# Performance work log

Measured on AMD Instinct MI355X. Metric: run time of the kernel, lower is better.

The kernel has to match this reference:

```python
import jax, jax.numpy as jnp
import numpy as np

N, D, R, B, K = 16384, 300, 10, 1024, 64


def setup_inputs() -> dict:
    key = jax.random.key(0)
    ks = jax.random.split(key, 6)
    return {
        "node_feat_src": jax.random.normal(ks[0], (N, D), jnp.float32),
        "node_feat_tgt": jax.random.normal(ks[1], (N, D), jnp.float32),
        "srcs_index": jax.random.randint(ks[2], (B, K), 0, N),
        "tgts_index": jax.random.randint(ks[3], (B, K), 0, N),
        "src_vs": jax.random.normal(ks[4], (R, D), jnp.float32),
        "tgt_vs": jax.random.normal(ks[5], (R, D), jnp.float32),
    }


def _tower(h, vs):
    # Householder chain: h @ (I - v v^T / (v^T v)) == h - ((h v) / (v^T v)) v^T
    def step(h, v):
        coef = (h @ v) / (v @ v)  # [N]
        return h - coef[:, None] * v[None, :], None
    h, _ = jax.lax.scan(step, h, vs)
    return h


def _l2norm(x):
    # matches F.normalize(p=2, eps=1e-12) over the last dim
    n = jnp.linalg.norm(x, axis=-1, keepdims=True)
    return x / jnp.maximum(n, 1e-12)


def reference(node_feat_src, node_feat_tgt, srcs_index, tgts_index, src_vs, tgt_vs):
    src_h = _tower(node_feat_src, src_vs)  # [N, D]
    tgt_h = _tower(node_feat_tgt, tgt_vs)  # [N, D]

    pos_src = _l2norm(src_h[srcs_index[:, 0]])  # [B, D]
    pos_tgt = _l2norm(tgt_h[tgts_index[:, 0]])  # [B, D]
    src_list = _l2norm(src_h[srcs_index])       # [B, K, D]
    tgt_list = _l2norm(tgt_h[tgts_index])       # [B, K, D]

    sim_src2tgt = jnp.einsum('bd,bkd->bk', pos_src, tgt_list)  # [B, K]
    sim_tgt2src = jnp.einsum('bd,bkd->bk', pos_tgt, src_list)  # [B, K]

    # CSLS hubness penalties: mean of top-10 cross-domain cosine sims
    sim_matrix = _l2norm(src_h) @ _l2norm(tgt_h).T  # [N, N]
    rt = jnp.mean(jax.lax.top_k(sim_matrix, 10)[0], axis=1)    # [N]
    rs = jnp.mean(jax.lax.top_k(sim_matrix.T, 10)[0], axis=1)  # [N]

    srcs_rt = rt[srcs_index]  # [B, K]
    tgts_rs = rs[tgts_index]  # [B, K]

    logits_src2tgt = sim_src2tgt * 2 - srcs_rt[:, 0:1] - tgts_rs
    logits_tgt2src = sim_tgt2src * 2 - tgts_rs[:, 0:1] - srcs_rt
    return logits_src2tgt, logits_tgt2src
```

## Files before the change

kernel.cpp:

```cpp
#include <hip/hip_runtime.h>
#include <hip/hip_bf16.h>

#define NN 16384
#define DD 300
#define DP 320
#define RR 10
#define BB 1024
#define KK 64
#define CAP 128
#define CAPL 1024

typedef __attribute__((ext_vector_type(8))) short s8v;
typedef __attribute__((ext_vector_type(4))) float f4v;
typedef _Float16 h2 __attribute__((ext_vector_type(2)));

__device__ __forceinline__ unsigned mono2(unsigned d) {
    unsigned s = ((d >> 15) & 0x10001u) * 0xFFFFu;
    return d ^ (s | 0x80008000u);
}
__device__ __forceinline__ float key2f16(unsigned k) {
    unsigned short b = (k & 0x8000u) ? (unsigned short)(k ^ 0x8000u)
                                     : (unsigned short)(~k & 0xFFFFu);
    _Float16 hv = __builtin_bit_cast(_Float16, b);
    return (float)hv;
}

__device__ __forceinline__ h2 h2max(h2 a, h2 b) {
    return __builtin_elementwise_max(a, b);
}
__device__ __forceinline__ h2 hmax2s(h2 a, int xb) {
    int x = __shfl_xor(__builtin_bit_cast(int, a), xb);
    return h2max(a, __builtin_bit_cast(h2, x));
}
__device__ __forceinline__ h2 packh2(float a, float b) {
    h2 r; r[0] = (_Float16)a; r[1] = (_Float16)b; return r;
}

__device__ __forceinline__ void ins10(unsigned (&lst)[10], unsigned v) {
    #pragma unroll
    for (int q = 0; q < 10; ++q) {
        unsigned a  = lst[q];
        unsigned mx = a > v ? a : v;
        v           = a > v ? v : a;
        lst[q] = mx;
    }
}
__device__ __forceinline__ void ins10f(float (&lst)[10], float v) {
    #pragma unroll
    for (int q = 0; q < 10; ++q) {
        float a  = lst[q];
        float mx = fmaxf(a, v);
        v        = fminf(a, v);
        lst[q] = mx;
    }
}

__device__ __forceinline__ void xcd_map(int bid, int& by, int& bx) {
    const int xcd = bid & 7;
    const int s   = bid >> 3;
    bx = (xcd << 2) | (s & 3);
    by = s >> 2;
}

__global__ __launch_bounds__(256) void tower_kernel(
        const float* __restrict__ feat, const float* __restrict__ vs,
        __hip_bfloat16* __restrict__ out) {
    __shared__ float vsh[RR * DD];
    const int tid = threadIdx.x;
    for (int i = tid; i < RR * DD; i += 256) vsh[i] = vs[i];
    __syncthreads();

    const int lane = tid & 63;
    const int wave = tid >> 6;
    const int row  = blockIdx.x * 4 + wave;

    float h[5];
    #pragma unroll
    for (int j = 0; j < 5; ++j) {
        int d = lane + 64 * j;
        h[j] = (d < DD) ? feat[(size_t)row * DD + d] : 0.f;
    }
    #pragma unroll
    for (int r = 0; r < RR; ++r) {
        float vl[5];
        float hv = 0.f, vv = 0.f;
        #pragma unroll
        for (int j = 0; j < 5; ++j) {
            int d = lane + 64 * j;
            float v = (d < DD) ? vsh[r * DD + d] : 0.f;
            vl[j] = v;
            hv += h[j] * v;
            vv += v * v;
        }
        #pragma unroll
        for (int o = 32; o; o >>= 1) {
            hv += __shfl_xor(hv, o);
            vv += __shfl_xor(vv, o);
        }
        float coef = hv / vv;
        #pragma unroll
        for (int j = 0; j < 5; ++j) h[j] -= coef * vl[j];
    }
    float nn = 0.f;
    #pragma unroll
    for (int j = 0; j < 5; ++j) nn += h[j] * h[j];
    #pragma unroll
    for (int o = 32; o; o >>= 1) nn += __shfl_xor(nn, o);
    float scale = 1.f / fmaxf(sqrtf(nn), 1e-12f);
    #pragma unroll
    for (int j = 0; j < 5; ++j) {
        int d = lane + 64 * j;
        float val = (d < DD) ? h[j] * scale : 0.f;
        out[(size_t)row * DP + d] = __float2bfloat16(val);
    }
}

__global__ __launch_bounds__(512, 2) void passA_kernel(
        const __hip_bfloat16* __restrict__ A, const __hip_bfloat16* __restrict__ Bm,
        unsigned short* __restrict__ rowsmax_g,
        unsigned short* __restrict__ colsmax_g) {
    __shared__ __align__(16) char u_lds[32768];
    __shared__ unsigned short rowsm[16][512];
    __shared__ unsigned short colsm[512][16];

    __hip_bfloat16* Asub = (__hip_bfloat16*)u_lds;
    __hip_bfloat16* Bsub = (__hip_bfloat16*)(u_lds + 16384);

    const int tid = threadIdx.x;
    const int lane = tid & 63;
    const int w = tid >> 6, wr = w >> 2, wc = w & 3;
    int by, bx; xcd_map(blockIdx.x, by, bx);
    const int i0 = by * 512, j0 = bx * 512;

    const int sr0 = tid >> 3, su0 = tid & 7;
    const int sp0 = (su0 ^ (sr0 & 7)) * 8;

    for (int ti = 0; ti < 4; ++ti) {
        for (int tj = 0; tj < 4; ++tj) {
            f4v acc[4][2];
            #pragma unroll
            for (int m = 0; m < 4; ++m)
                #pragma unroll
                for (int n = 0; n < 2; ++n)
                    acc[m][n] = (f4v){0.f, 0.f, 0.f, 0.f};

            const __hip_bfloat16* Ab = A  + (size_t)(i0 + ti * 128) * DP;
            const __hip_bfloat16* Bb = Bm + (size_t)(j0 + tj * 128) * DP;

            size_t go = (size_t)sr0 * DP + su0 * 8;
            int4 va0 = *reinterpret_cast<const int4*>(Ab + go);
            int4 vb0 = *reinterpret_cast<const int4*>(Bb + go);
            int4 va1 = *reinterpret_cast<const int4*>(Ab + go + (size_t)64 * DP);
            int4 vb1 = *reinterpret_cast<const int4*>(Bb + go + (size_t)64 * DP);

            #pragma unroll
            for (int kb = 0; kb < 5; ++kb) {
                __syncthreads();
                *reinterpret_cast<int4*>(Asub + sr0 * 64 + sp0)        = va0;
                *reinterpret_cast<int4*>(Bsub + sr0 * 64 + sp0)        = vb0;
                *reinterpret_cast<int4*>(Asub + (sr0 + 64) * 64 + sp0) = va1;
                *reinterpret_cast<int4*>(Bsub + (sr0 + 64) * 64 + sp0) = vb1;
                __syncthreads();
                if (kb < 4) {
                    go += 64;
                    va0 = *reinterpret_cast<const int4*>(Ab + go);
                    vb0 = *reinterpret_cast<const int4*>(Bb + go);
                    va1 = *reinterpret_cast<const int4*>(Ab + go + (size_t)64 * DP);
                    vb1 = *reinterpret_cast<const int4*>(Bb + go + (size_t)64 * DP);
                }
                #pragma unroll
                for (int ks = 0; ks < 2; ++ks) {
                    s8v af[4], bfv[2];
                    const int ulog = ks * 4 + (lane >> 4);
                    const int up   = ulog ^ (lane & 7);
                    #pragma unroll
                    for (int m = 0; m < 4; ++m) {
                        const int row = wr * 64 + m * 16 + (lane & 15);
                        af[m] = *reinterpret_cast<const s8v*>(Asub + row * 64 + up * 8);
                    }
                    #pragma unroll
                    for (int n = 0; n < 2; ++n) {
                        const int row = wc * 32 + n * 16 + (lane & 15);
                        bfv[n] = *reinterpret_cast<const s8v*>(Bsub + row * 64 + up * 8);
                    }
                    #pragma unroll
                    for (int m = 0; m < 4; ++m)
                        #pragma unroll
                        for (int n = 0; n < 2; ++n)
                            acc[m][n] = __builtin_amdgcn_mfma_f32_16x16x32_bf16(
                                af[m], bfv[n], acc[m][n], 0, 0, 0);
                }
            }

            #pragma unroll
            for (int m = 0; m < 4; ++m) {
                h2 a01 = h2max(packh2(acc[m][0][0], acc[m][0][1]),
                               packh2(acc[m][1][0], acc[m][1][1]));
                h2 a23 = h2max(packh2(acc[m][0][2], acc[m][0][3]),
                               packh2(acc[m][1][2], acc[m][1][3]));
                a01 = hmax2s(a01, 1); a23 = hmax2s(a23, 1);
                a01 = hmax2s(a01, 2); a23 = hmax2s(a23, 2);
                a01 = hmax2s(a01, 4); a23 = hmax2s(a23, 4);
                a01 = hmax2s(a01, 8); a23 = hmax2s(a23, 8);
                if ((lane & 15) == m * 4) {
                    const int rl = ti * 128 + wr * 64 + m * 16 + ((lane >> 4) << 2);
                    uint2 u = make_uint2(mono2(__builtin_bit_cast(unsigned, a01)),
                                         mono2(__builtin_bit_cast(unsigned, a23)));
                    *reinterpret_cast<uint2*>(&rowsm[tj * 4 + wc][rl]) = u;
                }
            }
            float rm[4][2];
            #pragma unroll
            for (int m = 0; m < 4; ++m) {
                rm[m][0] = fmaxf(fmaxf(acc[m][0][0], acc[m][0][1]),
                                 fmaxf(acc[m][0][2], acc[m][0][3]));
                rm[m][1] = fmaxf(fmaxf(acc[m][1][0], acc[m][1][1]),
                                 fmaxf(acc[m][1][2], acc[m][1][3]));
            }
            h2 c0 = packh2(fmaxf(rm[0][0], rm[1][0]), fmaxf(rm[2][0], rm[3][0]));
            h2 c1 = packh2(fmaxf(rm[0][1], rm[1][1]), fmaxf(rm[2][1], rm[3][1]));
            c0 = hmax2s(c0, 16); c1 = hmax2s(c1, 16);
            c0 = hmax2s(c0, 32); c1 = hmax2s(c1, 32);
            if ((lane >> 4) == 0) {
                const int s = ti * 4 + wr * 2;
                const int cb = tj * 128 + wc * 32 + (lane & 15);
                *reinterpret_cast<unsigned*>(&colsm[cb][s])      = mono2(__builtin_bit_cast(unsigned, c0));
                *reinterpret_cast<unsigned*>(&colsm[cb + 16][s]) = mono2(__builtin_bit_cast(unsigned, c1));
            }
        }
    }
    __syncthreads();
    {
        const int r = tid;
        unsigned short t16[16];
        #pragma unroll
        for (int s = 0; s < 16; ++s) t16[s] = rowsm[s][r];
        uint4 o0, o1;
        o0.x = t16[0] | ((unsigned)t16[1] << 16);  o0.y = t16[2] | ((unsigned)t16[3] << 16);
        o0.z = t16[4] | ((unsigned)t16[5] << 16);  o0.w = t16[6] | ((unsigned)t16[7] << 16);
        o1.x = t16[8] | ((unsigned)t16[9] << 16);  o1.y = t16[10] | ((unsigned)t16[11] << 16);
        o1.z = t16[12] | ((unsigned)t16[13] << 16); o1.w = t16[14] | ((unsigned)t16[15] << 16);
        uint4* rdst = reinterpret_cast<uint4*>(rowsmax_g + (size_t)(i0 + r) * 512 + bx * 16);
        rdst[0] = o0; rdst[1] = o1;
        uint4 q0 = *reinterpret_cast<uint4*>(&colsm[r][0]);
        uint4 q1 = *reinterpret_cast<uint4*>(&colsm[r][8]);
        uint4* cdst = reinterpret_cast<uint4*>(colsmax_g + (size_t)(j0 + r) * 512 + by * 16);
        cdst[0] = q0; cdst[1] = q1;
    }
}

__global__ __launch_bounds__(256) void thresh_kernel(
        const unsigned short* __restrict__ rowsmax_g,
        const unsigned short* __restrict__ colsmax_g,
        float* __restrict__ Tlb_row, float* __restrict__ Tlb_col,
        unsigned* __restrict__ rowcnt, unsigned* __restrict__ colcnt) {
    const int t = blockIdx.x * 256 + threadIdx.x;
    const bool isRow = t < NN;
    const int idx = isRow ? t : t - NN;
    const unsigned short* src = (isRow ? rowsmax_g : colsmax_g) + (size_t)idx * 512;

    unsigned lst[10];
    #pragma unroll
    for (int q = 0; q < 10; ++q) lst[q] = 0u;

    const uint4* p = reinterpret_cast<const uint4*>(src);
    for (int c = 0; c < 64; ++c) {
        uint4 q = p[c];
        unsigned v0 = q.x & 0xFFFFu, v1 = q.x >> 16;
        unsigned v2 = q.y & 0xFFFFu, v3 = q.y >> 16;
        unsigned v4 = q.z & 0xFFFFu, v5 = q.z >> 16;
        unsigned v6 = q.w & 0xFFFFu, v7 = q.w >> 16;
        unsigned g01 = v0 > v1 ? v0 : v1, g23 = v2 > v3 ? v2 : v3;
        unsigned g45 = v4 > v5 ? v4 : v5, g67 = v6 > v7 ? v6 : v7;
        unsigned ga = g01 > g23 ? g01 : g23, gb = g45 > g67 ? g45 : g67;
        unsigned g = ga > gb ? ga : gb;
        if (g > lst[9]) {
            if (v0 > lst[9]) ins10(lst, v0);
            if (v1 > lst[9]) ins10(lst, v1);
            if (v2 > lst[9]) ins10(lst, v2);
            if (v3 > lst[9]) ins10(lst, v3);
            if (v4 > lst[9]) ins10(lst, v4);
            if (v5 > lst[9]) ins10(lst, v5);
            if (v6 > lst[9]) ins10(lst, v6);
            if (v7 > lst[9]) ins10(lst, v7);
        }
    }
    float f = key2f16(lst[9]);
    float lb = f - fabsf(f) * 0.002f - 1e-6f;
    if (isRow) { Tlb_row[idx] = lb; rowcnt[idx] = 0u; }
    else       { Tlb_col[idx] = lb; colcnt[idx] = 0u; }
}

__global__ __launch_bounds__(512, 2) void passB_kernel(
        const __hip_bfloat16* __restrict__ A, const __hip_bfloat16* __restrict__ Bm,
        const float* __restrict__ Tlb_row, const float* __restrict__ Tlb_col,
        unsigned* __restrict__ rowcnt, unsigned* __restrict__ colcnt,
        float* __restrict__ rowbuf, float* __restrict__ colbuf) {
    __shared__ __align__(16) char u_lds[32768];
    __shared__ float Trow_s[512];
    __shared__ float Tcol_s[512];
    __shared__ unsigned scnt[2];
    __shared__ uint2 sbuf[2][CAPL];

    __hip_bfloat16* Asub = (__hip_bfloat16*)u_lds;
    __hip_bfloat16* Bsub = (__hip_bfloat16*)(u_lds + 16384);

    const int tid = threadIdx.x;
    const int lane = tid & 63;
    const int w = tid >> 6, wr = w >> 2, wc = w & 3;
    int by, bx; xcd_map(blockIdx.x, by, bx);
    const int i0 = by * 512, j0 = bx * 512;

    Trow_s[tid] = Tlb_row[i0 + tid];
    Tcol_s[tid] = Tlb_col[j0 + tid];
    if (tid < 2) scnt[tid] = 0u;
    __syncthreads();

    const int sr0 = tid >> 3, su0 = tid & 7;
    const int sp0 = (su0 ^ (sr0 & 7)) * 8;

    for (int ti = 0; ti < 4; ++ti) {
        float trmin = 1e30f;
        #pragma unroll
        for (int m = 0; m < 4; ++m)
            #pragma unroll
            for (int r = 0; r < 4; ++r)
                trmin = fminf(trmin, Trow_s[ti * 128 + wr * 64 + m * 16 + ((lane >> 4) << 2) + r]);

        for (int tj = 0; tj < 4; ++tj) {
            f4v acc[4][2];
            #pragma unroll
            for (int m = 0; m < 4; ++m)
                #pragma unroll
                for (int n = 0; n < 2; ++n)
                    acc[m][n] = (f4v){0.f, 0.f, 0.f, 0.f};

            const __hip_bfloat16* Ab = A  + (size_t)(i0 + ti * 128) * DP;
            const __hip_bfloat16* Bb = Bm + (size_t)(j0 + tj * 128) * DP;

            size_t go = (size_t)sr0 * DP + su0 * 8;
            int4 va0 = *reinterpret_cast<const int4*>(Ab + go);
            int4 vb0 = *reinterpret_cast<const int4*>(Bb + go);
            int4 va1 = *reinterpret_cast<const int4*>(Ab + go + (size_t)64 * DP);
            int4 vb1 = *reinterpret_cast<const int4*>(Bb + go + (size_t)64 * DP);

            #pragma unroll
            for (int kb = 0; kb < 5; ++kb) {
                __syncthreads();
                *reinterpret_cast<int4*>(Asub + sr0 * 64 + sp0)        = va0;
                *reinterpret_cast<int4*>(Bsub + sr0 * 64 + sp0)        = vb0;
                *reinterpret_cast<int4*>(Asub + (sr0 + 64) * 64 + sp0) = va1;
                *reinterpret_cast<int4*>(Bsub + (sr0 + 64) * 64 + sp0) = vb1;
                __syncthreads();
                if (kb < 4) {
                    go += 64;
                    va0 = *reinterpret_cast<const int4*>(Ab + go);
                    vb0 = *reinterpret_cast<const int4*>(Bb + go);
                    va1 = *reinterpret_cast<const int4*>(Ab + go + (size_t)64 * DP);
                    vb1 = *reinterpret_cast<const int4*>(Bb + go + (size_t)64 * DP);
                }
                #pragma unroll
                for (int ks = 0; ks < 2; ++ks) {
                    s8v af[4], bfv[2];
                    const int ulog = ks * 4 + (lane >> 4);
                    const int up   = ulog ^ (lane & 7);
                    #pragma unroll
                    for (int m = 0; m < 4; ++m) {
                        const int row = wr * 64 + m * 16 + (lane & 15);
                        af[m] = *reinterpret_cast<const s8v*>(Asub + row * 64 + up * 8);
                    }
                    #pragma unroll
                    for (int n = 0; n < 2; ++n) {
                        const int row = wc * 32 + n * 16 + (lane & 15);
                        bfv[n] = *reinterpret_cast<const s8v*>(Bsub + row * 64 + up * 8);
                    }
                    #pragma unroll
                    for (int m = 0; m < 4; ++m)
                        #pragma unroll
                        for (int n = 0; n < 2; ++n)
                            acc[m][n] = __builtin_amdgcn_mfma_f32_16x16x32_bf16(
                                af[m], bfv[n], acc[m][n], 0, 0, 0);
                }
            }

            const int c0i = tj * 128 + wc * 32 + (lane & 15);
            const int c1i = c0i + 16;
            const float tc0 = Tcol_s[c0i], tc1 = Tcol_s[c1i];
            float vm = -1e30f;
            #pragma unroll
            for (int m = 0; m < 4; ++m) {
                float a = fmaxf(fmaxf(acc[m][0][0], acc[m][0][1]),
                                fmaxf(acc[m][0][2], acc[m][0][3]));
                float b = fmaxf(fmaxf(acc[m][1][0], acc[m][1][1]),
                                fmaxf(acc[m][1][2], acc[m][1][3]));
                vm = fmaxf(vm, fmaxf(a, b));
            }
            if (vm >= fminf(trmin, fminf(tc0, tc1))) {
                #pragma unroll
                for (int m = 0; m < 4; ++m) {
                    #pragma unroll
                    for (int r = 0; r < 4; ++r) {
                        const int rl = ti * 128 + wr * 64 + m * 16 + ((lane >> 4) << 2) + r;
                        const float T = Trow_s[rl];
                        const float v0 = acc[m][0][r], v1 = acc[m][1][r];
                        if (v0 >= T) {
                            unsigned p = atomicAdd(&scnt[0], 1u);
                            if (p < CAPL) sbuf[0][p] = make_uint2((unsigned)(i0 + rl), __float_as_uint(v0));
                            else { unsigned q = atomicAdd(&rowcnt[i0 + rl], 1u);
                                   if (q < CAP) rowbuf[(size_t)(i0 + rl) * CAP + q] = v0; }
                        }
                        if (v1 >= T) {
                            unsigned p = atomicAdd(&scnt[0], 1u);
                            if (p < CAPL) sbuf[0][p] = make_uint2((unsigned)(i0 + rl), __float_as_uint(v1));
                            else { unsigned q = atomicAdd(&rowcnt[i0 + rl], 1u);
                                   if (q < CAP) rowbuf[(size_t)(i0 + rl) * CAP + q] = v1; }
                        }
                        if (v0 >= tc0) {
                            unsigned p = atomicAdd(&scnt[1], 1u);
                            if (p < CAPL) sbuf[1][p] = make_uint2((unsigned)(j0 + c0i), __float_as_uint(v0));
                            else { unsigned q = atomicAdd(&colcnt[j0 + c0i], 1u);
                                   if (q < CAP) colbuf[(size_t)(j0 + c0i) * CAP + q] = v0; }
                        }
                        if (v1 >= tc1) {
                            unsigned p = atomicAdd(&scnt[1], 1u);
                            if (p < CAPL) sbuf[1][p] = make_uint2((unsigned)(j0 + c1i), __float_as_uint(v1));
                            else { unsigned q = atomicAdd(&colcnt[j0 + c1i], 1u);
                                   if (q < CAP) colbuf[(size_t)(j0 + c1i) * CAP + q] = v1; }
                        }
                    }
                }
            }
        }
    }

    __syncthreads();
    {
        const unsigned nr = scnt[0] < CAPL ? scnt[0] : CAPL;
        const unsigned nc = scnt[1] < CAPL ? scnt[1] : CAPL;
        for (unsigned i = tid; i < nr; i += 512) {
            uint2 e = sbuf[0][i];
            unsigned p = atomicAdd(&rowcnt[e.x], 1u);
            if (p < CAP) rowbuf[(size_t)e.x * CAP + p] = __uint_as_float(e.y);
        }
        for (unsigned i = tid; i < nc; i += 512) {
            uint2 e = sbuf[1][i];
            unsigned p = atomicAdd(&colcnt[e.x], 1u);
            if (p < CAP) colbuf[(size_t)e.x * CAP + p] = __uint_as_float(e.y);
        }
    }
}

__global__ __launch_bounds__(256) void final_kernel(
        const unsigned* __restrict__ rowcnt, const unsigned* __restrict__ colcnt,
        const float* __restrict__ rowbuf, const float* __restrict__ colbuf,
        float* __restrict__ rt, float* __restrict__ rs) {
    const int t = blockIdx.x * 256 + threadIdx.x;
    const bool isRow = t < NN;
    const int idx = isRow ? t : t - NN;
    const unsigned cn = (isRow ? rowcnt : colcnt)[idx];
    const int n = (int)(cn < CAP ? cn : CAP);
    const float* buf = (isRow ? rowbuf : colbuf) + (size_t)idx * CAP;

    float lst[10];
    #pragma unroll
    for (int q = 0; q < 10; ++q) lst[q] = -1e30f;
    for (int i = 0; i < n; ++i) {
        float v = buf[i];
        if (v > lst[9]) ins10f(lst, v);
    }
    float s = 0.f;
    #pragma unroll
    for (int q = 0; q < 10; ++q) s += lst[q];
    s *= 0.1f;
    (isRow ? rt : rs)[idx] = s;
}

__global__ __launch_bounds__(256) void logits_kernel(
        const __hip_bfloat16* __restrict__ srcH, const __hip_bfloat16* __restrict__ tgtH,
        const int* __restrict__ sidx, const int* __restrict__ tidx,
        const float* __restrict__ rt, const float* __restrict__ rs,
        float* __restrict__ out) {
    const int b    = blockIdx.x;
    const int lane = threadIdx.x & 63;
    const int w    = threadIdx.x >> 6;

    const int s0 = sidx[b * KK];
    const int t0 = tidx[b * KK];
    float ps[5], pt[5];
    #pragma unroll
    for (int j = 0; j < 5; ++j) {
        int d = lane + 64 * j;
        ps[j] = __bfloat162float(srcH[(size_t)s0 * DP + d]);
        pt[j] = __bfloat162float(tgtH[(size_t)t0 * DP + d]);
    }
    const float rt_s0 = rt[s0];
    const float rs_t0 = rs[t0];

    for (int kk = w; kk < KK; kk += 4) {
        const int it = tidx[b * KK + kk];
        const int is = sidx[b * KK + kk];
        float a = 0.f, c = 0.f;
        #pragma unroll
        for (int j = 0; j < 5; ++j) {
            int d = lane + 64 * j;
            a += ps[j] * __bfloat162float(tgtH[(size_t)it * DP + d]);
            c += pt[j] * __bfloat162float(srcH[(size_t)is * DP + d]);
        }
        #pragma unroll
        for (int o = 32; o; o >>= 1) {
            a += __shfl_xor(a, o);
            c += __shfl_xor(c, o);
        }
        if (lane == 0) {
            out[b * KK + kk]           = 2.f * a - rt_s0 - rs[it];
            out[BB * KK + b * KK + kk] = 2.f * c - rs_t0 - rt[is];
        }
    }
}

extern "C" void kernel_launch(void* const* d_in, const int* in_sizes, int n_in,
                              void* d_out, int out_size, void* d_ws, size_t ws_size,
                              hipStream_t stream) {
    const float* nf_src = (const float*)d_in[0];
    const float* nf_tgt = (const float*)d_in[1];
    const int*   sidx   = (const int*)d_in[2];
    const int*   tidx   = (const int*)d_in[3];
    const float* svs    = (const float*)d_in[4];
    const float* tvs    = (const float*)d_in[5];

    char* ws = (char*)d_ws;
    const size_t SZ_H  = (size_t)NN * DP * 2;
    const size_t SZ_SM = (size_t)NN * 512 * 2;
    __hip_bfloat16* srcH = (__hip_bfloat16*)ws;
    __hip_bfloat16* tgtH = (__hip_bfloat16*)(ws + SZ_H);
    unsigned short* rowsmax = (unsigned short*)(ws + 2 * SZ_H);
    unsigned short* colsmax = (unsigned short*)(ws + 2 * SZ_H + SZ_SM);
    float* rowbuf = (float*)(ws + 2 * SZ_H);
    float* colbuf = (float*)(ws + 2 * SZ_H + (size_t)NN * CAP * 4);
    char* tail = ws + 2 * SZ_H + 2 * SZ_SM;
    float* Tlb_row = (float*)(tail);
    float* Tlb_col = (float*)(tail + 65536);
    unsigned* rowcnt = (unsigned*)(tail + 2 * 65536);
    unsigned* colcnt = (unsigned*)(tail + 3 * 65536);
    float* rt = (float*)(tail + 4 * 65536);
    float* rs = (float*)(tail + 5 * 65536);

    tower_kernel<<<NN / 4, 256, 0, stream>>>(nf_src, svs, srcH);
    tower_kernel<<<NN / 4, 256, 0, stream>>>(nf_tgt, tvs, tgtH);
    passA_kernel<<<1024, 512, 0, stream>>>(srcH, tgtH, rowsmax, colsmax);
    thresh_kernel<<<(2 * NN) / 256, 256, 0, stream>>>(rowsmax, colsmax, Tlb_row, Tlb_col,
                                                      rowcnt, colcnt);
    passB_kernel<<<1024, 512, 0, stream>>>(srcH, tgtH, Tlb_row, Tlb_col,
                                           rowcnt, colcnt, rowbuf, colbuf);
    final_kernel<<<(2 * NN) / 256, 256, 0, stream>>>(rowcnt, colcnt, rowbuf, colbuf, rt, rs);
    logits_kernel<<<BB, 256, 0, stream>>>(srcH, tgtH, sidx, tidx, rt, rs, (float*)d_out);
}
```

Measured before the change: 693.6 us.

## Stage GEMM tiles with direct global-to-LDS loads and raise occupancy

Both passes of the similarity GEMM now copy A/B tiles straight from global memory into LDS with the global_load_lds builtin, instead of staging through registers with a one-step register prefetch. Launch bounds rise to 4 blocks per CU, and the passB candidate buffer (CAPL) is halved so the LDS footprint fits more resident blocks. The intent is to cut VGPR pressure and the register-to-LDS copy instructions so more waves can hide latency. In exchange the explicit prefetch overlap is gone, because each load now sits between two barriers, and the smaller candidate buffer may overflow more often.

```diff
diff --git a/kernel.cpp b/kernel.cpp
--- a/kernel.cpp
+++ b/kernel.cpp
@@ -8,7 +8,7 @@
 #define BB 1024
 #define KK 64
 #define CAP 128
-#define CAPL 1024
+#define CAPL 512
 
 typedef __attribute__((ext_vector_type(8))) short s8v;
 typedef __attribute__((ext_vector_type(4))) float f4v;
@@ -60,6 +60,35 @@
     const int s   = bid >> 3;
     bx = (xcd << 2) | (s & 3);
     by = s >> 2;
+}
+
+__device__ __forceinline__ void gload_lds16(const void* g, void* l) {
+#if __has_builtin(__builtin_amdgcn_global_load_lds)
+    __builtin_amdgcn_global_load_lds(
+        (const __attribute__((address_space(1))) void*)g,
+        (__attribute__((address_space(3))) void*)l, 16, 0, 0);
+#else
+    const int lane = threadIdx.x & 63;
+    int4 v = *reinterpret_cast<const int4*>(g);
+    *reinterpret_cast<int4*>((char*)l + lane * 16) = v;
+#endif
+}
+
+__device__ __forceinline__ void stage_tile(
+        const __hip_bfloat16* __restrict__ Ab, const __hip_bfloat16* __restrict__ Bb,
+        int kb, char* lds, int w, int lane) {
+    const int r8 = lane >> 3;
+    const int u  = (lane & 7) ^ r8;
+    #pragma unroll
+    for (int q = 0; q < 4; ++q) {
+        const int chunk = q * 8 + w;
+        const int cm = chunk & 15;
+        const int row = cm * 8 + r8;
+        const __hip_bfloat16* src =
+            (chunk < 16 ? Ab : Bb) + (size_t)row * DP + kb * 64 + u * 8;
+        char* dst = lds + (chunk < 16 ? 0 : 16384) + cm * 1024;
+        gload_lds16(src, dst);
+    }
 }
 
 __global__ __launch_bounds__(256) void tower_kernel(
@@ -115,7 +144,7 @@
     }
 }
 
-__global__ __launch_bounds__(512, 2) void passA_kernel(
+__global__ __launch_bounds__(512, 4) void passA_kernel(
         const __hip_bfloat16* __restrict__ A, const __hip_bfloat16* __restrict__ Bm,
         unsigned short* __restrict__ rowsmax_g,
         unsigned short* __restrict__ colsmax_g) {
@@ -132,9 +161,6 @@
     int by, bx; xcd_map(blockIdx.x, by, bx);
     const int i0 = by * 512, j0 = bx * 512;
 
-    const int sr0 = tid >> 3, su0 = tid & 7;
-    const int sp0 = (su0 ^ (sr0 & 7)) * 8;
-
     for (int ti = 0; ti < 4; ++ti) {
         for (int tj = 0; tj < 4; ++tj) {
             f4v acc[4][2];
@@ -147,27 +173,11 @@
             const __hip_bfloat16* Ab = A  + (size_t)(i0 + ti * 128) * DP;
             const __hip_bfloat16* Bb = Bm + (size_t)(j0 + tj * 128) * DP;
 
-            size_t go = (size_t)sr0 * DP + su0 * 8;
-            int4 va0 = *reinterpret_cast<const int4*>(Ab + go);
-            int4 vb0 = *reinterpret_cast<const int4*>(Bb + go);
-            int4 va1 = *reinterpret_cast<const int4*>(Ab + go + (size_t)64 * DP);
-            int4 vb1 = *reinterpret_cast<const int4*>(Bb + go + (size_t)64 * DP);
-
             #pragma unroll
             for (int kb = 0; kb < 5; ++kb) {
                 __syncthreads();
-                *reinterpret_cast<int4*>(Asub + sr0 * 64 + sp0)        = va0;
-                *reinterpret_cast<int4*>(Bsub + sr0 * 64 + sp0)        = vb0;
-                *reinterpret_cast<int4*>(Asub + (sr0 + 64) * 64 + sp0) = va1;
-                *reinterpret_cast<int4*>(Bsub + (sr0 + 64) * 64 + sp0) = vb1;
+                stage_tile(Ab, Bb, kb, u_lds, w, lane);
                 __syncthreads();
-                if (kb < 4) {
-                    go += 64;
-                    va0 = *reinterpret_cast<const int4*>(Ab + go);
-                    vb0 = *reinterpret_cast<const int4*>(Bb + go);
-                    va1 = *reinterpret_cast<const int4*>(Ab + go + (size_t)64 * DP);
-                    vb1 = *reinterpret_cast<const int4*>(Bb + go + (size_t)64 * DP);
-                }
                 #pragma unroll
                 for (int ks = 0; ks < 2; ++ks) {
                     s8v af[4], bfv[2];
@@ -291,7 +301,7 @@
     else       { Tlb_col[idx] = lb; colcnt[idx] = 0u; }
 }
 
-__global__ __launch_bounds__(512, 2) void passB_kernel(
+__global__ __launch_bounds__(512, 4) void passB_kernel(
         const __hip_bfloat16* __restrict__ A, const __hip_bfloat16* __restrict__ Bm,
         const float* __restrict__ Tlb_row, const float* __restrict__ Tlb_col,
         unsigned* __restrict__ rowcnt, unsigned* __restrict__ colcnt,
@@ -316,9 +326,6 @@
     if (tid < 2) scnt[tid] = 0u;
     __syncthreads();
 
-    const int sr0 = tid >> 3, su0 = tid & 7;
-    const int sp0 = (su0 ^ (sr0 & 7)) * 8;
-
     for (int ti = 0; ti < 4; ++ti) {
         float trmin = 1e30f;
         #pragma unroll
@@ -338,27 +345,11 @@
             const __hip_bfloat16* Ab = A  + (size_t)(i0 + ti * 128) * DP;
             const __hip_bfloat16* Bb = Bm + (size_t)(j0 + tj * 128) * DP;
 
-            size_t go = (size_t)sr0 * DP + su0 * 8;
-            int4 va0 = *reinterpret_cast<const int4*>(Ab + go);
-            int4 vb0 = *reinterpret_cast<const int4*>(Bb + go);
-            int4 va1 = *reinterpret_cast<const int4*>(Ab + go + (size_t)64 * DP);
-            int4 vb1 = *reinterpret_cast<const int4*>(Bb + go + (size_t)64 * DP);
-
             #pragma unroll
             for (int kb = 0; kb < 5; ++kb) {
                 __syncthreads();
-                *reinterpret_cast<int4*>(Asub + sr0 * 64 + sp0)        = va0;
-                *reinterpret_cast<int4*>(Bsub + sr0 * 64 + sp0)        = vb0;
-                *reinterpret_cast<int4*>(Asub + (sr0 + 64) * 64 + sp0) = va1;
-                *reinterpret_cast<int4*>(Bsub + (sr0 + 64) * 64 + sp0) = vb1;
+                stage_tile(Ab, Bb, kb, u_lds, w, lane);
                 __syncthreads();
-                if (kb < 4) {
-                    go += 64;
-                    va0 = *reinterpret_cast<const int4*>(Ab + go);
-                    vb0 = *reinterpret_cast<const int4*>(Bb + go);
-                    va1 = *reinterpret_cast<const int4*>(Ab + go + (size_t)64 * DP);
-                    vb1 = *reinterpret_cast<const int4*>(Bb + go + (size_t)64 * DP);
-                }
                 #pragma unroll
                 for (int ks = 0; ks < 2; ++ks) {
                     s8v af[4], bfv[2];
```

New measurement: 670.8 us. -3.3%, faster.
